# Kernel optimization log

Hardware: AMD Instinct MI355X
Metric: run time of the kernel (lower is better)

## Reference

```python
import jax, jax.numpy as jnp
import numpy as np

DIM = 768
HEADS = 12
DIM_HEAD = 64
INNER = HEADS * DIM_HEAD  # 768
N = 197  # num_patches + 1
B = 64


def setup_inputs() -> dict:
    key = jax.random.key(0)
    k0, k1, k2, k3, k4 = jax.random.split(key, 5)
    x = jax.random.normal(k0, (B, N, DIM), dtype=jnp.float32)
    # Linear weights stored as [in, out] for x @ W
    W_qkv = jax.random.normal(k1, (DIM, 3 * INNER), dtype=jnp.float32) * (1.0 / np.sqrt(DIM))
    W_out = jax.random.normal(k2, (INNER, DIM), dtype=jnp.float32) * (1.0 / np.sqrt(INNER))
    b_out = jnp.zeros((DIM,), dtype=jnp.float32)
    scale = jnp.full((HEADS,), DIM_HEAD ** -0.5, dtype=jnp.float32)
    return {"x": x, "scale": scale, "W_qkv": W_qkv, "W_out": W_out, "b_out": b_out}


def reference(x, scale, W_qkv, W_out, b_out):
    b, n, _ = x.shape
    qkv = x @ W_qkv  # [b, n, 3*inner]
    q, k, v = jnp.split(qkv, 3, axis=-1)
    def to_heads(t):
        return t.reshape(b, n, HEADS, DIM_HEAD).transpose(0, 2, 1, 3)  # b h n d
    q, k, v = to_heads(q), to_heads(k), to_heads(v)
    # per-head learnable scale applied to raw dot products
    dots = jnp.einsum('bhid,bhjd->bhij', q, k) * scale[None, :, None, None]
    # diagonal self-mask: set dots[i,i] = -inf before softmax
    diag = jnp.eye(n, dtype=bool)[None, None]
    dots = jnp.where(diag, -jnp.inf, dots)
    attn = jax.nn.softmax(dots, axis=-1)
    out = jnp.einsum('bhij,bhjd->bhid', attn, v)
    out = out.transpose(0, 2, 1, 3).reshape(b, n, INNER)
    return out @ W_out + b_out
```

## Files before the change

### kernel.cpp

```cpp
#include <hip/hip_runtime.h>
#include <hip/hip_bf16.h>

typedef __attribute__((ext_vector_type(8))) short short8;
typedef __attribute__((ext_vector_type(4))) float floatx4;

#define MFMA_BF16(a, b, c) __builtin_amdgcn_mfma_f32_16x16x32_bf16((a), (b), (c), 0, 0, 0)

__device__ __forceinline__ unsigned short f2bf(float f) {
    union { float f; unsigned u; } v; v.f = f;
    unsigned r = v.u + 0x7fffu + ((v.u >> 16) & 1u);
    return (unsigned short)(r >> 16);
}

__device__ __forceinline__ void gload16(const unsigned short* g, unsigned short* l) {
    __builtin_amdgcn_global_load_lds(
        (const __attribute__((address_space(1))) unsigned int*)g,
        (__attribute__((address_space(3))) unsigned int*)l, 16, 0, 0);
}

__global__ void cast_f32_to_bf16(const float* __restrict__ src,
                                 unsigned short* __restrict__ dst, int n4) {
    int i = blockIdx.x * blockDim.x + threadIdx.x;
    int stride = gridDim.x * blockDim.x;
    for (; i < n4; i += stride) {
        float4 f = reinterpret_cast<const float4*>(src)[i];
        ushort4 o;
        o.x = f2bf(f.x); o.y = f2bf(f.y); o.z = f2bf(f.z); o.w = f2bf(f.w);
        reinterpret_cast<ushort4*>(dst)[i] = o;
    }
}

__global__ void transpose_cast(const float* __restrict__ src,
                               unsigned short* __restrict__ dst, int R, int C) {
    __shared__ float tile[32][33];
    int c0 = blockIdx.x * 32, r0 = blockIdx.y * 32;
    int tx = threadIdx.x, ty = threadIdx.y;
#pragma unroll
    for (int i = 0; i < 32; i += 8)
        tile[ty + i][tx] = src[(long)(r0 + ty + i) * C + (c0 + tx)];
    __syncthreads();
#pragma unroll
    for (int i = 0; i < 32; i += 8)
        dst[(long)(c0 + ty + i) * R + (r0 + tx)] = f2bf(tile[tx][ty + i]);
}

template <bool OUT_BF16>
__global__ __launch_bounds__(256, 4) void gemm_bt(
    const unsigned short* __restrict__ A,
    const unsigned short* __restrict__ B,
    void* __restrict__ Cout,
    const float* __restrict__ bias,
    int M, int N, int K) {
    __shared__ __align__(16) unsigned short Alds[128 * 64];
    __shared__ __align__(16) unsigned short Blds[128 * 64];

    int tid = threadIdx.x;
    int lane = tid & 63, wave = tid >> 6;
    int m0 = blockIdx.y * 128, n0 = blockIdx.x * 128;
    int wm = (wave >> 1) * 64, wn = (wave & 1) * 64;

    floatx4 acc[4][4];
#pragma unroll
    for (int mi = 0; mi < 4; mi++)
#pragma unroll
        for (int ni = 0; ni < 4; ni++) acc[mi][ni] = (floatx4){0.f, 0.f, 0.f, 0.f};

    int srow = tid >> 3;
    int scol = (((tid & 7) ^ (srow & 7)) << 3);
    const unsigned short* ap[4];
    const unsigned short* bp[4];
    unsigned short* la[4];
    unsigned short* lb[4];
#pragma unroll
    for (int i = 0; i < 4; i++) {
        int row = i * 32 + srow;
        int ar = m0 + row; if (ar >= M) ar = M - 1;
        ap[i] = A + (long)ar * K + scol;
        bp[i] = B + (long)(n0 + row) * K + scol;
        la[i] = &Alds[row * 64 + (tid & 7) * 8];
        lb[i] = &Blds[row * 64 + (tid & 7) * 8];
    }

    for (int k0 = 0; k0 < K; k0 += 64) {
        __syncthreads();
#pragma unroll
        for (int i = 0; i < 4; i++) gload16(ap[i] + k0, la[i]);
#pragma unroll
        for (int i = 0; i < 4; i++) gload16(bp[i] + k0, lb[i]);
        __syncthreads();

#pragma unroll
        for (int ks = 0; ks < 2; ks++) {
            int sw = ((ks * 4 + (lane >> 4)) ^ (lane & 7)) * 8;
            short8 af[4], bfr[4];
#pragma unroll
            for (int mi = 0; mi < 4; mi++)
                af[mi] = *reinterpret_cast<const short8*>(
                    &Alds[(wm + mi * 16 + (lane & 15)) * 64 + sw]);
#pragma unroll
            for (int ni = 0; ni < 4; ni++)
                bfr[ni] = *reinterpret_cast<const short8*>(
                    &Blds[(wn + ni * 16 + (lane & 15)) * 64 + sw]);
#pragma unroll
            for (int mi = 0; mi < 4; mi++)
#pragma unroll
                for (int ni = 0; ni < 4; ni++)
                    acc[mi][ni] = MFMA_BF16(af[mi], bfr[ni], acc[mi][ni]);
        }
    }

    if (OUT_BF16) {
        unsigned short* C = (unsigned short*)Cout;
#pragma unroll
        for (int mi = 0; mi < 4; mi++)
#pragma unroll
            for (int rr = 0; rr < 4; rr++) {
                int row = m0 + wm + mi * 16 + (lane >> 4) * 4 + rr;
                if (row < M) {
                    long rbase = (long)row * N + n0 + wn + (lane & 15);
#pragma unroll
                    for (int ni = 0; ni < 4; ni++)
                        C[rbase + ni * 16] = f2bf(acc[mi][ni][rr]);
                }
            }
    } else {
        float* C = (float*)Cout;
        float bv[4];
#pragma unroll
        for (int ni = 0; ni < 4; ni++) bv[ni] = bias[n0 + wn + ni * 16 + (lane & 15)];
#pragma unroll
        for (int mi = 0; mi < 4; mi++)
#pragma unroll
            for (int rr = 0; rr < 4; rr++) {
                int row = m0 + wm + mi * 16 + (lane >> 4) * 4 + rr;
                if (row < M) {
                    long rbase = (long)row * N + n0 + wn + (lane & 15);
#pragma unroll
                    for (int ni = 0; ni < 4; ni++)
                        C[rbase + ni * 16] = acc[mi][ni][rr] + bv[ni];
                }
            }
    }
}

__global__ __launch_bounds__(448, 2) void attn_kernel(
    const unsigned short* __restrict__ qkv,
    const float* __restrict__ scale,
    unsigned short* __restrict__ out) {
    const int N = 197, D3 = 2304;
    const int NT = 13;
    int b = blockIdx.x / 12, h = blockIdx.x % 12;
    int tid = threadIdx.x, lane = tid & 63, wave = tid >> 6;

    __shared__ __align__(16) unsigned short Klds[208 * 64];
    __shared__ __align__(16) unsigned short Vlds[64 * 224];
    __shared__ __align__(16) unsigned short Plds[7 * 16 * 32];

    const unsigned short* base = qkv + (long)b * N * D3 + h * 64;

    for (int idx = tid; idx < 208 * 8; idx += 448) {
        int r = idx >> 3, s = idx & 7;
        short8 v = {0, 0, 0, 0, 0, 0, 0, 0};
        if (r < N) v = *reinterpret_cast<const short8*>(base + (long)r * D3 + 768 + s * 8);
        *reinterpret_cast<short8*>(&Klds[r * 64 + (s ^ (r & 7)) * 8]) = v;
    }
    for (int idx = tid; idx < 224 * 8; idx += 448) {
        int j = idx >> 3, sg = idx & 7;
        short8 v = {0, 0, 0, 0, 0, 0, 0, 0};
        if (j < N) v = *reinterpret_cast<const short8*>(base + (long)j * D3 + 1536 + sg * 8);
        int s = j >> 3;
#pragma unroll
        for (int e = 0; e < 8; e++) {
            int d = sg * 8 + e;
            Vlds[d * 224 + (s ^ (d & 3)) * 8 + (j & 7)] = (unsigned short)v[e];
        }
    }
    __syncthreads();

    float sc = scale[h];
    unsigned short* Pw = &Plds[wave * (16 * 32)];

    for (int rtb = 0; rtb < 2; rtb++) {
        int rt = wave + rtb * 7;
        int i0 = rt * 16;
        int qrow = i0 + (lane & 15); if (qrow > N - 1) qrow = N - 1;
        const unsigned short* qp = base + (long)qrow * D3;
        short8 qf[2];
#pragma unroll
        for (int kb = 0; kb < 2; kb++)
            qf[kb] = *reinterpret_cast<const short8*>(qp + kb * 32 + (lane >> 4) * 8);

        floatx4 sf[NT];
#pragma unroll
        for (int jt = 0; jt < NT; jt++) sf[jt] = (floatx4){0.f, 0.f, 0.f, 0.f};
#pragma unroll
        for (int jt = 0; jt < NT; jt++) {
#pragma unroll
            for (int kb = 0; kb < 2; kb++) {
                int r = jt * 16 + (lane & 15);
                int slot = kb * 4 + (lane >> 4);
                short8 kf = *reinterpret_cast<const short8*>(
                    &Klds[r * 64 + (slot ^ (r & 7)) * 8]);
                sf[jt] = MFMA_BF16(qf[kb], kf, sf[jt]);
            }
        }

        int rowg[4];
        float mx[4], sm[4];
#pragma unroll
        for (int rr = 0; rr < 4; rr++) { rowg[rr] = i0 + (lane >> 4) * 4 + rr; mx[rr] = -1e30f; }
#pragma unroll
        for (int jt = 0; jt < NT; jt++) {
            int col = jt * 16 + (lane & 15);
#pragma unroll
            for (int rr = 0; rr < 4; rr++) {
                float v = sf[jt][rr] * sc;
                if (col >= N || col == rowg[rr]) v = -1e30f;
                sf[jt][rr] = v;
                mx[rr] = fmaxf(mx[rr], v);
            }
        }
#pragma unroll
        for (int rr = 0; rr < 4; rr++) {
#pragma unroll
            for (int m = 1; m <= 8; m <<= 1)
                mx[rr] = fmaxf(mx[rr], __shfl_xor(mx[rr], m, 64));
            sm[rr] = 0.f;
        }
#pragma unroll
        for (int jt = 0; jt < NT; jt++)
#pragma unroll
            for (int rr = 0; rr < 4; rr++) {
                float p = __expf(sf[jt][rr] - mx[rr]);
                sf[jt][rr] = p;
                sm[rr] += p;
            }
#pragma unroll
        for (int rr = 0; rr < 4; rr++)
#pragma unroll
            for (int m = 1; m <= 8; m <<= 1)
                sm[rr] += __shfl_xor(sm[rr], m, 64);

        floatx4 oacc[4];
#pragma unroll
        for (int dt = 0; dt < 4; dt++) oacc[dt] = (floatx4){0.f, 0.f, 0.f, 0.f};
#pragma unroll
        for (int c = 0; c < 7; c++) {
#pragma unroll
            for (int jh = 0; jh < 2; jh++) {
                int jtc = c * 2 + jh;
#pragma unroll
                for (int rr = 0; rr < 4; rr++) {
                    int row = (lane >> 4) * 4 + rr;
                    int jj = jh * 16 + (lane & 15);
                    float pv = (jtc < NT) ? sf[jtc < NT ? jtc : 0][rr] : 0.f;
                    Pw[row * 32 + ((jj >> 3) ^ (row & 3)) * 8 + (jj & 7)] = f2bf(pv);
                }
            }
            int prow = lane & 15;
            short8 pa = *reinterpret_cast<const short8*>(
                &Pw[prow * 32 + (((lane >> 4)) ^ (prow & 3)) * 8]);
#pragma unroll
            for (int dt = 0; dt < 4; dt++) {
                int d = dt * 16 + (lane & 15);
                int slot = c * 4 + (lane >> 4);
                short8 vf = *reinterpret_cast<const short8*>(
                    &Vlds[d * 224 + (slot ^ (d & 3)) * 8]);
                oacc[dt] = MFMA_BF16(pa, vf, oacc[dt]);
            }
        }

#pragma unroll
        for (int rr = 0; rr < 4; rr++) {
            int n = rowg[rr];
            if (n < N) {
                float r = 1.f / sm[rr];
                long o = ((long)b * N + n) * 768 + h * 64;
#pragma unroll
                for (int dt = 0; dt < 4; dt++)
                    out[o + dt * 16 + (lane & 15)] = f2bf(oacc[dt][rr] * r);
            }
        }
    }
}

extern "C" void kernel_launch(void* const* d_in, const int* in_sizes, int n_in,
                              void* d_out, int out_size, void* d_ws, size_t ws_size,
                              hipStream_t stream) {
    (void)in_sizes; (void)n_in; (void)out_size; (void)ws_size;
    const float* x     = (const float*)d_in[0];
    const float* scale = (const float*)d_in[1];
    const float* Wqkv  = (const float*)d_in[2];
    const float* Wout  = (const float*)d_in[3];
    const float* bout  = (const float*)d_in[4];
    float* out = (float*)d_out;

    const int M = 12608;
    char* ws = (char*)d_ws;
    unsigned short* x_bf   = (unsigned short*)(ws);
    unsigned short* wqkv_t = (unsigned short*)(ws + 19365888);
    unsigned short* wout_t = (unsigned short*)(ws + 22904832);
    unsigned short* qkv    = (unsigned short*)(ws + 24084480);
    unsigned short* ao     = (unsigned short*)(ws + 82182144);

    cast_f32_to_bf16<<<2048, 256, 0, stream>>>(x, x_bf, (M * 768) / 4);
    transpose_cast<<<dim3(2304 / 32, 768 / 32), dim3(32, 8), 0, stream>>>(Wqkv, wqkv_t, 768, 2304);
    transpose_cast<<<dim3(768 / 32, 768 / 32), dim3(32, 8), 0, stream>>>(Wout, wout_t, 768, 768);
    gemm_bt<true><<<dim3(2304 / 128, 99), 256, 0, stream>>>(x_bf, wqkv_t, qkv, nullptr, M, 2304, 768);
    attn_kernel<<<768, 448, 0, stream>>>(qkv, scale, ao);
    gemm_bt<false><<<dim3(768 / 128, 99), 256, 0, stream>>>(ao, wout_t, out, bout, M, 768, 768);
}
```

Before: 204.7 us.

## Replace QKV GEMM with 256x256-tile 8-wave phased pipelined kernel

Adds a new GEMM kernel for the QKV projection using 256x256 output tiles, 8 waves, 128KB dynamic LDS with double buffering and XOR swizzle. Each k-step is split into four barrier-separated phases that interleave LDS fragment reads, next-tile global-to-LDS loads and MFMA bursts under raised wave priority. The aim is to overlap memory and compute and raise data reuse per tile. In exchange, the larger tiles leave fewer blocks (9x50) on the device, and the tail tiles past M use clamped rows.

New measurement: 215.3 us. 5.2% more time.

```diff
diff --git a/kernel.cpp b/kernel.cpp
--- a/kernel.cpp
+++ b/kernel.cpp
@@ -16,6 +16,12 @@
     __builtin_amdgcn_global_load_lds(
         (const __attribute__((address_space(1))) unsigned int*)g,
         (__attribute__((address_space(3))) unsigned int*)l, 16, 0, 0);
+}
+
+__device__ __forceinline__ void phase_barrier() {
+    __builtin_amdgcn_sched_barrier(0);
+    __builtin_amdgcn_s_barrier();
+    __builtin_amdgcn_sched_barrier(0);
 }
 
 __global__ void cast_f32_to_bf16(const float* __restrict__ src,
@@ -42,6 +48,158 @@
 #pragma unroll
     for (int i = 0; i < 32; i += 8)
         dst[(long)(c0 + ty + i) * R + (r0 + tx)] = f2bf(tile[tx][ty + i]);
+}
+
+__global__ __launch_bounds__(512, 2) void gemm_bt_8ph(
+    const unsigned short* __restrict__ A,
+    const unsigned short* __restrict__ B,
+    unsigned short* __restrict__ C,
+    int M, int N, int K) {
+    extern __shared__ unsigned short smem[];
+    unsigned short* Al = smem;
+    unsigned short* Bl = smem + 32768;
+
+    const int tid = threadIdx.x;
+    const int w = tid >> 6, lane = tid & 63;
+    const int fr = lane & 15, fq = lane >> 4;
+    const int swz = fr & 7;
+    const int wr = (w >> 2) * 64;
+    const int wc = (w & 3) * 32;
+    const int m0 = blockIdx.y * 256, n0 = blockIdx.x * 256;
+    const int T = K >> 6;
+
+    const int sr = (w << 4) + (lane >> 3);
+    const int ssl = lane & 7;
+    const int swsrc = ((ssl ^ (sr & 7)) << 3);
+
+    const unsigned short* gpA[2][2];
+    const unsigned short* gpB[2][2];
+    int lo[2][2];
+#pragma unroll
+    for (int h = 0; h < 2; h++)
+#pragma unroll
+        for (int s = 0; s < 2; s++) {
+            int ra = m0 + h * 128 + sr + s * 8; if (ra >= M) ra = M - 1;
+            int rb = n0 + h * 128 + sr + s * 8; if (rb >= N) rb = N - 1;
+            gpA[h][s] = A + (long)ra * K + swsrc;
+            gpB[h][s] = B + (long)rb * K + swsrc;
+            lo[h][s] = (h * 128 + sr + s * 8) * 64 + ssl * 8;
+        }
+
+#define STG_A(buf, h, kt) do { \
+    gload16(gpA[h][0] + (kt) * 64, Al + (buf) * 16384 + lo[h][0]); \
+    gload16(gpA[h][1] + (kt) * 64, Al + (buf) * 16384 + lo[h][1]); } while (0)
+#define STG_B(buf, h, kt) do { \
+    gload16(gpB[h][0] + (kt) * 64, Bl + (buf) * 16384 + lo[h][0]); \
+    gload16(gpB[h][1] + (kt) * 64, Bl + (buf) * 16384 + lo[h][1]); } while (0)
+#define DSA(mh, mi, ks) (*reinterpret_cast<const short8*>( \
+    &Ap[((mh) * 128 + wr + (mi) * 16 + fr) * 64 + ((((ks) * 4 + fq) ^ swz) * 8)]))
+#define DSB(nh, ni, ks) (*reinterpret_cast<const short8*>( \
+    &Bp[((nh) * 128 + wc + (ni) * 16 + fr) * 64 + ((((ks) * 4 + fq) ^ swz) * 8)]))
+
+    floatx4 acc[8][4];
+#pragma unroll
+    for (int i = 0; i < 8; i++)
+#pragma unroll
+        for (int j = 0; j < 4; j++) acc[i][j] = (floatx4){0.f, 0.f, 0.f, 0.f};
+
+    STG_A(0, 0, 0); STG_A(0, 1, 0); STG_B(0, 0, 0); STG_B(0, 1, 0);
+    STG_A(1, 0, 1); STG_B(1, 0, 1);
+    __builtin_amdgcn_sched_barrier(0);
+    asm volatile("s_waitcnt vmcnt(4)" ::: "memory");
+    phase_barrier();
+
+    for (int kt = 0; kt < T; ++kt) {
+        const int p = kt & 1, pn = p ^ 1;
+        const unsigned short* Ap = Al + p * 16384;
+        const unsigned short* Bp = Bl + p * 16384;
+        short8 af[4][2], bf0[2][2], bf1[2][2];
+
+#pragma unroll
+        for (int mi = 0; mi < 4; mi++) { af[mi][0] = DSA(0, mi, 0); af[mi][1] = DSA(0, mi, 1); }
+#pragma unroll
+        for (int ni = 0; ni < 2; ni++) { bf0[ni][0] = DSB(0, ni, 0); bf0[ni][1] = DSB(0, ni, 1); }
+        if (kt + 1 < T) STG_A(pn, 1, kt + 1);
+        phase_barrier();
+        __builtin_amdgcn_s_setprio(1);
+#pragma unroll
+        for (int mi = 0; mi < 4; mi++)
+#pragma unroll
+            for (int ni = 0; ni < 2; ni++) {
+                acc[mi][ni] = MFMA_BF16(af[mi][0], bf0[ni][0], acc[mi][ni]);
+                acc[mi][ni] = MFMA_BF16(af[mi][1], bf0[ni][1], acc[mi][ni]);
+            }
+        __builtin_amdgcn_s_setprio(0);
+        phase_barrier();
+
+#pragma unroll
+        for (int ni = 0; ni < 2; ni++) { bf1[ni][0] = DSB(1, ni, 0); bf1[ni][1] = DSB(1, ni, 1); }
+        if (kt + 1 < T) STG_B(pn, 1, kt + 1);
+        phase_barrier();
+        __builtin_amdgcn_s_setprio(1);
+#pragma unroll
+        for (int mi = 0; mi < 4; mi++)
+#pragma unroll
+            for (int ni = 0; ni < 2; ni++) {
+                acc[mi][2 + ni] = MFMA_BF16(af[mi][0], bf1[ni][0], acc[mi][2 + ni]);
+                acc[mi][2 + ni] = MFMA_BF16(af[mi][1], bf1[ni][1], acc[mi][2 + ni]);
+            }
+        __builtin_amdgcn_s_setprio(0);
+        phase_barrier();
+
+#pragma unroll
+        for (int mi = 0; mi < 4; mi++) { af[mi][0] = DSA(1, mi, 0); af[mi][1] = DSA(1, mi, 1); }
+        if (kt + 2 < T) STG_A(p, 0, kt + 2);
+        phase_barrier();
+        __builtin_amdgcn_s_setprio(1);
+#pragma unroll
+        for (int mi = 0; mi < 4; mi++)
+#pragma unroll
+            for (int ni = 0; ni < 2; ni++) {
+                acc[4 + mi][2 + ni] = MFMA_BF16(af[mi][0], bf1[ni][0], acc[4 + mi][2 + ni]);
+                acc[4 + mi][2 + ni] = MFMA_BF16(af[mi][1], bf1[ni][1], acc[4 + mi][2 + ni]);
+            }
+        __builtin_amdgcn_s_setprio(0);
+        phase_barrier();
+
+        if (kt + 2 < T) STG_B(p, 0, kt + 2);
+        phase_barrier();
+        __builtin_amdgcn_s_setprio(1);
+#pragma unroll
+        for (int mi = 0; mi < 4; mi++)
+#pragma unroll
+            for (int ni = 0; ni < 2; ni++) {
+                acc[4 + mi][ni] = MFMA_BF16(af[mi][0], bf0[ni][0], acc[4 + mi][ni]);
+                acc[4 + mi][ni] = MFMA_BF16(af[mi][1], bf0[ni][1], acc[4 + mi][ni]);
+            }
+        __builtin_amdgcn_s_setprio(0);
+        __builtin_amdgcn_sched_barrier(0);
+        if (kt + 2 < T) asm volatile("s_waitcnt vmcnt(4)" ::: "memory");
+        else            asm volatile("s_waitcnt vmcnt(0)" ::: "memory");
+        phase_barrier();
+    }
+
+#pragma unroll
+    for (int mh = 0; mh < 2; mh++)
+#pragma unroll
+        for (int mi = 0; mi < 4; mi++)
+#pragma unroll
+            for (int rr = 0; rr < 4; rr++) {
+                int row = m0 + mh * 128 + wr + mi * 16 + fq * 4 + rr;
+                if (row < M) {
+                    long rbase = (long)row * N + n0 + wc + fr;
+#pragma unroll
+                    for (int nh = 0; nh < 2; nh++)
+#pragma unroll
+                        for (int ni = 0; ni < 2; ni++)
+                            C[rbase + nh * 128 + ni * 16] =
+                                f2bf(acc[mh * 4 + mi][nh * 2 + ni][rr]);
+                }
+            }
+#undef STG_A
+#undef STG_B
+#undef DSA
+#undef DSB
 }
 
 template <bool OUT_BF16>
@@ -303,10 +461,13 @@
     unsigned short* qkv    = (unsigned short*)(ws + 24084480);
     unsigned short* ao     = (unsigned short*)(ws + 82182144);
 
+    hipFuncSetAttribute((const void*)gemm_bt_8ph,
+                        hipFuncAttributeMaxDynamicSharedMemorySize, 131072);
+
     cast_f32_to_bf16<<<2048, 256, 0, stream>>>(x, x_bf, (M * 768) / 4);
     transpose_cast<<<dim3(2304 / 32, 768 / 32), dim3(32, 8), 0, stream>>>(Wqkv, wqkv_t, 768, 2304);
     transpose_cast<<<dim3(768 / 32, 768 / 32), dim3(32, 8), 0, stream>>>(Wout, wout_t, 768, 768);
-    gemm_bt<true><<<dim3(2304 / 128, 99), 256, 0, stream>>>(x_bf, wqkv_t, qkv, nullptr, M, 2304, 768);
+    gemm_bt_8ph<<<dim3(2304 / 256, 50), 512, 131072, stream>>>(x_bf, wqkv_t, qkv, M, 2304, 768);
     attn_kernel<<<768, 448, 0, stream>>>(qkv, scale, ao);
     gemm_bt<false><<<dim3(768 / 128, 99), 256, 0, stream>>>(ao, wout_t, out, bout, M, 768, 768);
 }
```
